# Performance work log

Hardware: AMD Instinct MI355X
Metric: run time of the kernel (lower is better)

## Reference

```python
import jax, jax.numpy as jnp
import numpy as np

N, C, T, V = 32, 64, 256, 25   # batch, channels, frames, joints
REL, OUT, K = 8, 64, 5         # rel_channels = C//8, out_channels, 5 topology branches
NU = 17                        # upper-body joints (lower = V - NU = 8)


def setup_inputs() -> dict:
    key = jax.random.key(0)
    ks = jax.random.split(key, 8)
    sC = np.float32(1.0 / np.sqrt(C))
    sR = np.float32(1.0 / np.sqrt(REL))
    return {
        "x": jax.random.normal(ks[0], (N, C, T, V), jnp.float32),
        "A": jax.random.uniform(ks[1], (K, V, V), jnp.float32),
        # stacked 1x1-conv weights for the 5 branches (conv{k}_1_1, _1_2, _2, _3, _4)
        "W11": jax.random.normal(ks[2], (K, REL, C), jnp.float32) * sC,
        "b11": jnp.zeros((K, REL), jnp.float32),
        "W12": jax.random.normal(ks[3], (K, REL, C), jnp.float32) * sC,
        "b12": jnp.zeros((K, REL), jnp.float32),
        "W2": jax.random.normal(ks[4], (K, REL, C), jnp.float32) * sC,
        "b2": jnp.zeros((K, REL), jnp.float32),
        "W3": jax.random.normal(ks[5], (K, OUT, C), jnp.float32) * sC,
        "b3": jnp.zeros((K, OUT), jnp.float32),
        "W4": jax.random.normal(ks[6], (K, OUT, REL), jnp.float32) * sR,
        "b4": jnp.zeros((K, OUT), jnp.float32),
    }


def reference(x, A, W11, b11, W12, b12, W2, b2, W3, b3, W4, b4):
    # 1x1 conv followed by mean over T commutes with the (linear) conv:
    # conv(x).mean(T) == W @ x.mean(T) + b. Pool once, reuse across branches.
    mu = jnp.mean(x[:, :, :, :NU], axis=2)   # (N, C, 17)
    ml = jnp.mean(x[:, :, :, NU:], axis=2)   # (N, C, 8)

    u11 = jnp.einsum('krc,ncv->knrv', W11, mu) + b11[:, None, :, None]  # (K,N,R,17)
    u2 = jnp.einsum('krc,ncv->knrv', W2, mu) + b2[:, None, :, None]     # (K,N,R,17)
    l12 = jnp.einsum('krc,ncv->knrv', W12, ml) + b12[:, None, :, None]  # (K,N,R,8)
    l2 = jnp.einsum('krc,ncv->knrv', W2, ml) + b2[:, None, :, None]     # (K,N,R,8)

    # pairwise-difference topology blocks
    x_a = jnp.tanh(u11[..., :, None] - u2[..., None, :])   # (K,N,R,17,17)
    x_b = jnp.tanh(u11[..., :, None] - l2[..., None, :])   # (K,N,R,17,8)
    x_c = jnp.tanh(l12[..., :, None] - u2[..., None, :])   # (K,N,R,8,17)
    x_d = jnp.tanh(l12[..., :, None] - l2[..., None, :])   # (K,N,R,8,8)

    up = jnp.concatenate([x_a, x_b], axis=-1)   # (K,N,R,17,25)
    lo = jnp.concatenate([x_c, x_d], axis=-1)   # (K,N,R,8,25)

    # the original rotates the upper blocks: branch k uses upper from branch (k+1)%5
    up_rot = jnp.concatenate([up[1:], up[:1]], axis=0)
    full = jnp.concatenate([up_rot, lo], axis=-2)  # (K,N,R,25,25)

    graphs = jnp.einsum('kor,knruv->knouv', W4, full) + b4[:, None, :, None, None]  # (K,N,O,25,25)

    alpha = jnp.ones((K,), jnp.float32)  # default branch scales
    g = graphs * alpha[:, None, None, None, None] + A[:, None, None, :, :]

    x2 = jnp.einsum('koc,nctv->knotv', W3, x) + b3[:, None, :, None, None]  # (K,N,O,T,25)
    out = jnp.einsum('knouv,knotv->notu', g, x2)  # summed over the 5 branches
    return out, graphs
```

## Files before the change

kernel.cpp:

```cpp
#include <hip/hip_runtime.h>
#include <cstdint>
#include <cstddef>

#define N_  32
#define C_  64
#define T_  256
#define V_  25
#define R_  8
#define O_  64
#define K_  5
#define NU_ 17
#define U_  25
#define CV  (C_ * V_)
#define KC  32
#define NCH (CV / KC)
#define OG  4
#define NB  (OG * 32)

#define OUT_ELEMS ((size_t)N_ * O_ * T_ * V_)

typedef __attribute__((ext_vector_type(8))) short bf16x8;
typedef __attribute__((ext_vector_type(4))) float f32x4;

static __device__ __forceinline__ unsigned short f2bf(float f) {
    union { float f; unsigned u; } c; c.f = f;
    return (unsigned short)((c.u + 0x8000u) >> 16);
}
static __device__ __forceinline__ float bf2f(unsigned short h) {
    union { unsigned u; float f; } c; c.u = ((unsigned)h) << 16; return c.f;
}
static __device__ __forceinline__ unsigned pk2(float a, float b) {
    union { float f; unsigned u; } ca, cb; ca.f = a; cb.f = b;
    return ((ca.u + 0x8000u) >> 16) | ((cb.u + 0x8000u) & 0xFFFF0000u);
}

__global__ void k_xcast(const float* __restrict__ x, unsigned short* __restrict__ xT3,
                        float* __restrict__ pp) {
    __shared__ unsigned short tile[C_][408];
    int bid = blockIdx.x;
    int n = bid >> 4, tb = bid & 15;
    int tid = threadIdx.x;
    const float* xb = x + (size_t)n * C_ * T_ * V_ + tb * 400;
#pragma unroll
    for (int it = 0; it < 25; ++it) {
        int i = it * 256 + tid;
        int c = i / 100, q = i - c * 100;
        float4 v4 = *(const float4*)(xb + (size_t)c * (T_ * V_) + q * 4);
        uint2 w;
        w.x = pk2(v4.x, v4.y);
        w.y = pk2(v4.z, v4.w);
        *(uint2*)&tile[c][q * 4] = w;
    }
    __syncthreads();
    unsigned short* dstb = xT3 + ((size_t)(n * 16 + tb) * 200) * 128;
    for (int i = tid; i < 200 * 16; i += 256) {
        int sp = i >> 4, tl = i & 15;
        int v = sp >> 3, c0 = (sp & 7) * 8;
        unsigned short h[8];
#pragma unroll
        for (int j = 0; j < 8; ++j) h[j] = tile[c0 + j][tl * 25 + v];
        uint4 pk;
        pk.x = (unsigned)h[0] | ((unsigned)h[1] << 16);
        pk.y = (unsigned)h[2] | ((unsigned)h[3] << 16);
        pk.z = (unsigned)h[4] | ((unsigned)h[5] << 16);
        pk.w = (unsigned)h[6] | ((unsigned)h[7] << 16);
        *(uint4*)(dstb + (size_t)sp * 128 + tl * 8) = pk;
    }
    float* ppd = pp + ((size_t)n * 16 + tb) * CV;
    for (int e = tid; e < CV; e += 256) {
        int c = e / 25, v = e - c * 25;
        float s = 0.f;
#pragma unroll
        for (int t = 0; t < 16; ++t) s += bf2f(tile[c][t * 25 + v]);
        ppd[e] = s;
    }
}

__global__ void k_pool(const float* __restrict__ x, float* __restrict__ pool) {
    int nc = blockIdx.x;
    int t  = threadIdx.x;
    const float* px = x + ((size_t)nc * T_ + t) * V_;
    float acc[V_];
#pragma unroll
    for (int v = 0; v < V_; ++v) acc[v] = px[v];
#pragma unroll
    for (int off = 32; off > 0; off >>= 1) {
#pragma unroll
        for (int v = 0; v < V_; ++v) acc[v] += __shfl_down(acc[v], off, 64);
    }
    __shared__ float sm[4][V_];
    int wave = t >> 6, lane = t & 63;
    if (lane == 0) {
#pragma unroll
        for (int v = 0; v < V_; ++v) sm[wave][v] = acc[v];
    }
    __syncthreads();
    if (t < V_) {
        float s = sm[0][t] + sm[1][t] + sm[2][t] + sm[3][t];
        pool[(size_t)nc * V_ + t] = s * (1.0f / T_);
    }
}

__global__ void k_tvals(const float* __restrict__ pool,
                        const float* __restrict__ W11, const float* __restrict__ b11,
                        const float* __restrict__ W12, const float* __restrict__ b12,
                        const float* __restrict__ W2,  const float* __restrict__ b2,
                        float* __restrict__ t2o, float* __restrict__ tSo) {
    int kn = blockIdx.x;
    int k = kn / N_, n = kn % N_;
    int tid = threadIdx.x;
    int r = tid >> 5, v = tid & 31;
    if (v >= V_) return;
    const float* pp = pool + (size_t)n * C_ * V_ + v;
    const float* w2 = W2 + ((size_t)k * R_ + r) * C_;
    const float* w1 = ((v < NU_) ? W11 : W12) + ((size_t)k * R_ + r) * C_;
    float a2 = b2[k * R_ + r];
    float a1 = (v < NU_) ? b11[k * R_ + r] : b12[k * R_ + r];
    for (int c = 0; c < C_; ++c) {
        float p = pp[(size_t)c * V_];
        a2 += w2[c] * p;
        a1 += w1[c] * p;
    }
    size_t idx = (((size_t)k * N_ + n) * R_ + r) * V_ + v;
    t2o[idx] = a2;
    tSo[idx] = a1;
}

__global__ void k_graphs(const float* __restrict__ t2v, const float* __restrict__ tSv,
                         const float* __restrict__ W4, const float* __restrict__ b4,
                         float* __restrict__ graphs) {
    int kn = blockIdx.x;
    int k = kn / N_, n = kn % N_;
    int kup = (k + 1) % K_;
    __shared__ float F[R_][V_ * V_];
    __shared__ float w4s[O_][R_];
    __shared__ float b4s[O_];
    int tid = threadIdx.x;
    for (int i = tid; i < O_ * R_; i += 256) w4s[i / R_][i % R_] = W4[(size_t)k * O_ * R_ + i];
    if (tid < O_) b4s[tid] = b4[k * O_ + tid];
    for (int idx = tid; idx < R_ * V_ * V_; idx += 256) {
        int r = idx / (V_ * V_), uv = idx % (V_ * V_);
        int u = uv / V_, v = uv % V_;
        int ks = (u < NU_) ? kup : k;
        size_t base = (((size_t)ks * N_ + n) * R_ + r) * V_;
        F[r][uv] = tanhf(tSv[base + u] - t2v[base + v]);
    }
    __syncthreads();
    float* gout = graphs + ((size_t)k * N_ + n) * O_ * (V_ * V_);
    for (int idx = tid; idx < O_ * V_ * V_; idx += 256) {
        int o = idx / (V_ * V_), uv = idx % (V_ * V_);
        float a = b4s[o];
#pragma unroll
        for (int r = 0; r < R_; ++r) a += w4s[o][r] * F[r][uv];
        gout[idx] = a;
    }
}

__global__ void k_graphs2b(const float* __restrict__ pp,
                           const float* __restrict__ W11, const float* __restrict__ b11,
                           const float* __restrict__ W12, const float* __restrict__ b12,
                           const float* __restrict__ W2,  const float* __restrict__ b2,
                           const float* __restrict__ W4,  const float* __restrict__ b4,
                           float* __restrict__ graphs) {
    int kn = blockIdx.x;
    int k = kn / N_, n = kn % N_;
    int kup = (k + 1) % K_;
    __shared__ float poolL[CV];
    __shared__ float t2s[2][R_][V_];
    __shared__ float tSs[2][R_][V_];
    __shared__ float F[R_][V_ * V_];
    __shared__ float w4s[O_][R_];
    __shared__ float b4s[O_];
    int tid = threadIdx.x;
    for (int i = tid; i < O_ * R_; i += 512) w4s[i / R_][i % R_] = W4[(size_t)k * O_ * R_ + i];
    if (tid < O_) b4s[tid] = b4[k * O_ + tid];
    const float* ppn = pp + (size_t)n * 16 * CV;
    for (int i = tid; i < CV; i += 512) {
        float s = 0.f;
#pragma unroll
        for (int tb = 0; tb < 16; ++tb) s += ppn[(size_t)tb * CV + i];
        poolL[i] = s * (1.0f / T_);
    }
    __syncthreads();
    for (int i = tid; i < 2 * R_ * V_; i += 512) {
        int ks = i / (R_ * V_);
        int rem = i - ks * (R_ * V_);
        int r = rem / V_, v = rem - r * V_;
        int kk = ks ? kup : k;
        const float* w2 = W2 + ((size_t)kk * R_ + r) * C_;
        const float* w1 = ((v < NU_) ? W11 : W12) + ((size_t)kk * R_ + r) * C_;
        float a2 = b2[kk * R_ + r];
        float a1 = (v < NU_) ? b11[kk * R_ + r] : b12[kk * R_ + r];
        for (int c = 0; c < C_; ++c) {
            float p = poolL[c * 25 + v];
            a2 += w2[c] * p;
            a1 += w1[c] * p;
        }
        t2s[ks][r][v] = a2;
        tSs[ks][r][v] = a1;
    }
    __syncthreads();
    for (int idx = tid; idx < R_ * V_ * V_; idx += 512) {
        int r = idx / (V_ * V_), uv = idx % (V_ * V_);
        int u = uv / V_, v = uv % V_;
        int ks = (u < NU_) ? 1 : 0;
        F[r][uv] = tanhf(tSs[ks][r][u] - t2s[ks][r][v]);
    }
    __syncthreads();
    float* gout = graphs + ((size_t)k * N_ + n) * O_ * (V_ * V_);
    for (int idx = tid; idx < O_ * V_ * V_; idx += 512) {
        int o = idx / (V_ * V_), uv = idx % (V_ * V_);
        float a = b4s[o];
#pragma unroll
        for (int r = 0; r < R_; ++r) a += w4s[o][r] * F[r][uv];
        gout[idx] = a;
    }
}

__global__ __launch_bounds__(512, 4) void k_main_fast(
    const unsigned short* __restrict__ xT3,
    const float* __restrict__ graphs,
    const float* __restrict__ Adj,
    const float* __restrict__ W3,
    const float* __restrict__ b3,
    float* __restrict__ out) {

    __shared__ unsigned short Hs[2][4][NB][8];
    __shared__ f32x4 Gls4[OG * 625];
    __shared__ float Gls1[OG * 625];
    __shared__ f32x4 W3km[K_ * OG * 16];
    __shared__ float biasS[NB];

    const int tid = threadIdx.x;
    const int bid = blockIdx.x;
    const int obase = (bid & 15) * OG;
    const int n = bid >> 4;
    const int lane = tid & 63;
    const int wv_ = tid >> 6;

    const size_t kstride = (size_t)N_ * O_ * 625;
    for (int i = tid; i < OG * 625; i += 512) {
        int o = i / 625, uv = i - o * 625;
        int u = uv / 25, v = uv - u * 25;
        size_t gb = ((size_t)n * O_ + obase + o) * 625 + uv;
        f32x4 g4;
        g4[0] = graphs[gb]               + Adj[uv];
        g4[1] = graphs[gb + kstride]     + Adj[625 + uv];
        g4[2] = graphs[gb + 2 * kstride] + Adj[1250 + uv];
        g4[3] = graphs[gb + 3 * kstride] + Adj[1875 + uv];
        int idx = o * 625 + v * 25 + u;
        Gls4[idx] = g4;
        Gls1[idx] = graphs[gb + 4 * kstride] + Adj[2500 + uv];
    }
    for (int i = tid; i < K_ * OG * C_; i += 512) {
        int k = i / (OG * C_);
        int rem = i - k * (OG * C_);
        int o = rem >> 6, c = rem & 63;
        ((float*)W3km)[((k * OG + o) * C_) + c] = W3[((size_t)k * O_ + obase + o) * C_ + c];
    }
    __syncthreads();

    if (tid < NB) {
        int o = tid >> 5, u = tid & 31;
        float bv = 0.f;
        if (u < U_) {
            f32x4 s4 = {0.f, 0.f, 0.f, 0.f};
            float s5 = 0.f;
            for (int v = 0; v < V_; ++v) {
                int idx = o * 625 + v * 25 + u;
                s4 += Gls4[idx];
                s5 += Gls1[idx];
            }
            bv = s4[0] * b3[0 * O_ + obase + o] + s4[1] * b3[1 * O_ + obase + o]
               + s4[2] * b3[2 * O_ + obase + o] + s4[3] * b3[3 * O_ + obase + o]
               + s5 * b3[4 * O_ + obase + o];
        }
        biasS[tid] = bv;
    }

    const int sl = wv_ & 3;
    const int hncol = (wv_ >> 2) * 64 + lane;
    const int ho = hncol >> 5;
    const int hu = hncol & 31;
    auto h_form = [&](int buf, int kc) {
        const int v  = kc >> 1;
        const int c0 = (kc & 1) * 32 + sl * 8;
        f32x4 g = {0.f, 0.f, 0.f, 0.f};
        float g5 = 0.f;
        if (hu < U_) {
            int gi = ho * 625 + v * 25 + hu;
            g = Gls4[gi];
            g5 = Gls1[gi];
        }
        const f32x4* wb = &W3km[(ho * 16) + (c0 >> 2)];
        const int kw = OG * 16;
        f32x4 w0a = wb[0],        w0b = wb[1];
        f32x4 w1a = wb[kw],       w1b = wb[kw + 1];
        f32x4 w2a = wb[2 * kw],   w2b = wb[2 * kw + 1];
        f32x4 w3a = wb[3 * kw],   w3b = wb[3 * kw + 1];
        f32x4 w4a = wb[4 * kw],   w4b = wb[4 * kw + 1];
        float h[8];
#pragma unroll
        for (int j = 0; j < 4; ++j) {
            h[j]     = w0a[j] * g[0] + w1a[j] * g[1] + w2a[j] * g[2] + w3a[j] * g[3] + w4a[j] * g5;
            h[4 + j] = w0b[j] * g[0] + w1b[j] * g[1] + w2b[j] * g[2] + w3b[j] * g[3] + w4b[j] * g5;
        }
        uint4 hv;
        hv.x = pk2(h[0], h[1]); hv.y = pk2(h[2], h[3]);
        hv.z = pk2(h[4], h[5]); hv.w = pk2(h[6], h[7]);
        *(uint4*)&Hs[buf][sl][hncol][0] = hv;
    };

    const int wm = wv_ >> 1;
    const int wn = wv_ & 1;
    const int lr = lane & 15;
    const int eg = lane >> 4;

    f32x4 acc[4][4];
#pragma unroll
    for (int mt = 0; mt < 4; ++mt)
#pragma unroll
        for (int nt = 0; nt < 4; ++nt) acc[mt][nt] = (f32x4){0.f, 0.f, 0.f, 0.f};

    h_form(0, 0);
    __syncthreads();

    const unsigned short* An = xT3 + (size_t)n * (T_ * CV);

    for (int kc = 0; kc < NCH; ++kc) {
        const int cur = kc & 1;
        uint4 av[4];
#pragma unroll
        for (int mt = 0; mt < 4; ++mt) {
            int tt = wm * 4 + mt;
            av[mt] = *(const uint4*)(An + ((size_t)(tt * 200 + kc * 4 + eg)) * 128 + lr * 8);
        }
        bf16x8 b[4];
#pragma unroll
        for (int nt = 0; nt < 4; ++nt)
            b[nt] = *(const bf16x8*)&Hs[cur][eg][wn * 64 + nt * 16 + lr][0];
        __builtin_amdgcn_s_setprio(1);
#pragma unroll
        for (int mt = 0; mt < 4; ++mt) {
            bf16x8 a;
            { union { uint4 u; bf16x8 h; } cvt; cvt.u = av[mt]; a = cvt.h; }
#pragma unroll
            for (int nt = 0; nt < 4; ++nt)
                acc[mt][nt] = __builtin_amdgcn_mfma_f32_16x16x32_bf16(a, b[nt], acc[mt][nt], 0, 0, 0);
        }
        __builtin_amdgcn_s_setprio(0);
        if (kc + 1 < NCH) h_form(cur ^ 1, kc + 1);
        __syncthreads();
    }

#pragma unroll
    for (int nt = 0; nt < 4; ++nt) {
        int ncol = wn * 64 + nt * 16 + lr;
        int ol = ncol >> 5;
        int u  = ncol & 31;
        if (u < U_) {
            float bv = biasS[ncol];
            float* ob = out + ((size_t)n * O_ + obase + ol) * T_ * V_ + u;
#pragma unroll
            for (int mt = 0; mt < 4; ++mt) {
                int t0 = wm * 64 + mt * 16 + eg * 4;
#pragma unroll
                for (int r2 = 0; r2 < 4; ++r2)
                    ob[(size_t)(t0 + r2) * V_] = acc[mt][nt][r2] + bv;
            }
        }
    }
}

#define OB 4
#define TB 64
__global__ __launch_bounds__(256, 1) void k_main_slow(
    const float* __restrict__ x, const float* __restrict__ graphs,
    const float* __restrict__ A, const float* __restrict__ W3,
    const float* __restrict__ b3, float* __restrict__ out) {
    int bid = blockIdx.x;
    int tb = bid & 3;
    int ob = (bid >> 2) & 15;
    int n  = bid >> 6;
    int tid = threadIdx.x;
    int ol = tid >> 6;
    int tl = tid & 63;
    int t = tb * TB + tl;
    int o = ob * OB + ol;

    __shared__ float Gs[K_][OB][V_][28];
    __shared__ float W3s[K_][OB][C_];
    __shared__ float b3s[K_][OB];

    for (int i = tid; i < K_ * OB * V_ * V_; i += 256) {
        int k   = i / (OB * V_ * V_);
        int rem = i % (OB * V_ * V_);
        int oo  = rem / (V_ * V_);
        int uv  = rem % (V_ * V_);
        Gs[k][oo][uv / V_][uv % V_] =
            graphs[(((size_t)k * N_ + n) * O_ + ob * OB + oo) * (V_ * V_) + uv]
            + A[k * V_ * V_ + uv];
    }
    for (int i = tid; i < K_ * OB * C_; i += 256) {
        int k   = i / (OB * C_);
        int rem = i % (OB * C_);
        int oo  = rem / C_, c = rem % C_;
        W3s[k][oo][c] = W3[((size_t)k * O_ + ob * OB + oo) * C_ + c];
    }
    if (tid < K_ * OB) b3s[tid / OB][tid % OB] = b3[(tid / OB) * O_ + ob * OB + tid % OB];
    __syncthreads();

    float x2[K_][V_];
#pragma unroll
    for (int k = 0; k < K_; ++k)
#pragma unroll
        for (int v = 0; v < V_; ++v) x2[k][v] = b3s[k][ol];

    const float* xb = x + ((size_t)n * C_ * T_ + t) * V_;
    for (int c = 0; c < C_; ++c) {
        const float* p = xb + (size_t)c * T_ * V_;
        float xv[V_];
#pragma unroll
        for (int v = 0; v < V_; ++v) xv[v] = p[v];
#pragma unroll
        for (int k = 0; k < K_; ++k) {
            float w = W3s[k][ol][c];
#pragma unroll
            for (int v = 0; v < V_; ++v) x2[k][v] += w * xv[v];
        }
    }

    float acc[V_];
#pragma unroll
    for (int u = 0; u < V_; ++u) acc[u] = 0.0f;
#pragma unroll
    for (int k = 0; k < K_; ++k) {
#pragma unroll
        for (int u = 0; u < V_; ++u) {
            const float* gr = &Gs[k][ol][u][0];
            float s = 0.0f;
#pragma unroll
            for (int v = 0; v < V_; ++v) s += gr[v] * x2[k][v];
            acc[u] += s;
        }
    }
    float* po = out + (((size_t)n * O_ + o) * T_ + t) * V_;
#pragma unroll
    for (int u = 0; u < V_; ++u) po[u] = acc[u];
}

extern "C" void kernel_launch(void* const* d_in, const int* in_sizes, int n_in,
                              void* d_out, int out_size, void* d_ws, size_t ws_size,
                              hipStream_t stream) {
    const float* x   = (const float*)d_in[0];
    const float* A   = (const float*)d_in[1];
    const float* W11 = (const float*)d_in[2];
    const float* b11 = (const float*)d_in[3];
    const float* W12 = (const float*)d_in[4];
    const float* b12 = (const float*)d_in[5];
    const float* W2  = (const float*)d_in[6];
    const float* b2  = (const float*)d_in[7];
    const float* W3  = (const float*)d_in[8];
    const float* b3  = (const float*)d_in[9];
    const float* W4  = (const float*)d_in[10];
    const float* b4  = (const float*)d_in[11];

    float* out    = (float*)d_out;
    float* graphs = out + OUT_ELEMS;

    const size_t xT_bytes = sizeof(unsigned short) * (size_t)N_ * T_ * CV;
    const size_t pp_bytes = sizeof(float) * (size_t)N_ * 16 * CV;
    const size_t hdr      = (size_t)(1 << 20);
    const bool fast = (ws_size >= hdr + xT_bytes + pp_bytes);

    const size_t poolElems = (size_t)N_ * C_ * V_;
    const size_t tElems    = (size_t)K_ * N_ * R_ * V_;
    const size_t slowNeed  = (poolElems + 2 * tElems) * sizeof(float);

    float* scratch = (fast || ws_size >= slowNeed) ? (float*)d_ws : out;
    float* pool = scratch;
    float* t2v  = scratch + poolElems;
    float* tSv  = t2v + tElems;
    unsigned short* xT3 = (unsigned short*)((char*)d_ws + hdr);
    float* pp = (float*)((char*)d_ws + hdr + xT_bytes);

    if (fast) {
        k_xcast   <<<N_ * 16, 256, 0, stream>>>(x, xT3, pp);
        k_graphs2b<<<K_ * N_, 512, 0, stream>>>(pp, W11, b11, W12, b12, W2, b2, W4, b4, graphs);
        k_main_fast<<<N_ * 16, 512, 0, stream>>>(xT3, graphs, A, W3, b3, out);
    } else {
        k_pool  <<<N_ * C_, 256, 0, stream>>>(x, pool);
        k_tvals <<<K_ * N_, 256, 0, stream>>>(pool, W11, b11, W12, b12, W2, b2, t2v, tSv);
        k_graphs<<<K_ * N_, 256, 0, stream>>>(t2v, tSv, W4, b4, graphs);
        k_main_slow<<<N_ * (O_ / OB) * 4, 256, 0, stream>>>(x, graphs, A, W3, b3, out);
    }
}
```

Measured before the change: 116.1 us.

## Process two K-chunks per barrier with quad-buffered H and bf16 graphs in LDS

The main GEMM loop now handles two joint chunks between barriers, using four H slots instead of two. This cuts the number of __syncthreads from about 50 to 26 per block. The combined graph+adjacency tiles are stored in LDS as packed bf16 rather than fp32, which halves that footprint to make room for the larger H buffer. The cost is an extra rounding of G to bf16 before H is formed, with a small accuracy risk, plus some unpacking ALU work.

```diff
diff --git a/kernel.cpp b/kernel.cpp
--- a/kernel.cpp
+++ b/kernel.cpp
@@ -12,8 +12,6 @@
 #define NU_ 17
 #define U_  25
 #define CV  (C_ * V_)
-#define KC  32
-#define NCH (CV / KC)
 #define OG  4
 #define NB  (OG * 32)
 
@@ -28,6 +26,12 @@
 }
 static __device__ __forceinline__ float bf2f(unsigned short h) {
     union { unsigned u; float f; } c; c.u = ((unsigned)h) << 16; return c.f;
+}
+static __device__ __forceinline__ float bf_lo(unsigned d) {
+    union { unsigned u; float f; } c; c.u = d << 16; return c.f;
+}
+static __device__ __forceinline__ float bf_hi(unsigned d) {
+    union { unsigned u; float f; } c; c.u = d & 0xFFFF0000u; return c.f;
 }
 static __device__ __forceinline__ unsigned pk2(float a, float b) {
     union { float f; unsigned u; } ca, cb; ca.f = a; cb.f = b;
@@ -225,9 +229,9 @@
     const float* __restrict__ b3,
     float* __restrict__ out) {
 
-    __shared__ unsigned short Hs[2][4][NB][8];
-    __shared__ f32x4 Gls4[OG * 625];
-    __shared__ float Gls1[OG * 625];
+    __shared__ unsigned short Hs[4][4][NB][8];
+    __shared__ uint2 Gbf4[OG * 625];
+    __shared__ unsigned short Gbf1[OG * 625];
     __shared__ f32x4 W3km[K_ * OG * 16];
     __shared__ float biasS[NB];
 
@@ -243,14 +247,15 @@
         int o = i / 625, uv = i - o * 625;
         int u = uv / 25, v = uv - u * 25;
         size_t gb = ((size_t)n * O_ + obase + o) * 625 + uv;
-        f32x4 g4;
-        g4[0] = graphs[gb]               + Adj[uv];
-        g4[1] = graphs[gb + kstride]     + Adj[625 + uv];
-        g4[2] = graphs[gb + 2 * kstride] + Adj[1250 + uv];
-        g4[3] = graphs[gb + 3 * kstride] + Adj[1875 + uv];
+        float g0 = graphs[gb]               + Adj[uv];
+        float g1 = graphs[gb + kstride]     + Adj[625 + uv];
+        float g2 = graphs[gb + 2 * kstride] + Adj[1250 + uv];
+        float g3 = graphs[gb + 3 * kstride] + Adj[1875 + uv];
+        float g4 = graphs[gb + 4 * kstride] + Adj[2500 + uv];
         int idx = o * 625 + v * 25 + u;
-        Gls4[idx] = g4;
-        Gls1[idx] = graphs[gb + 4 * kstride] + Adj[2500 + uv];
+        uint2 w; w.x = pk2(g0, g1); w.y = pk2(g2, g3);
+        Gbf4[idx] = w;
+        Gbf1[idx] = f2bf(g4);
     }
     for (int i = tid; i < K_ * OG * C_; i += 512) {
         int k = i / (OG * C_);
@@ -264,16 +269,17 @@
         int o = tid >> 5, u = tid & 31;
         float bv = 0.f;
         if (u < U_) {
-            f32x4 s4 = {0.f, 0.f, 0.f, 0.f};
-            float s5 = 0.f;
+            float s0 = 0.f, s1 = 0.f, s2 = 0.f, s3 = 0.f, s4 = 0.f;
             for (int v = 0; v < V_; ++v) {
                 int idx = o * 625 + v * 25 + u;
-                s4 += Gls4[idx];
-                s5 += Gls1[idx];
+                uint2 w = Gbf4[idx];
+                s0 += bf_lo(w.x); s1 += bf_hi(w.x);
+                s2 += bf_lo(w.y); s3 += bf_hi(w.y);
+                s4 += bf2f(Gbf1[idx]);
             }
-            bv = s4[0] * b3[0 * O_ + obase + o] + s4[1] * b3[1 * O_ + obase + o]
-               + s4[2] * b3[2 * O_ + obase + o] + s4[3] * b3[3 * O_ + obase + o]
-               + s5 * b3[4 * O_ + obase + o];
+            bv = s0 * b3[0 * O_ + obase + o] + s1 * b3[1 * O_ + obase + o]
+               + s2 * b3[2 * O_ + obase + o] + s3 * b3[3 * O_ + obase + o]
+               + s4 * b3[4 * O_ + obase + o];
         }
         biasS[tid] = bv;
     }
@@ -282,33 +288,40 @@
     const int hncol = (wv_ >> 2) * 64 + lane;
     const int ho = hncol >> 5;
     const int hu = hncol & 31;
-    auto h_form = [&](int buf, int kc) {
-        const int v  = kc >> 1;
-        const int c0 = (kc & 1) * 32 + sl * 8;
-        f32x4 g = {0.f, 0.f, 0.f, 0.f};
-        float g5 = 0.f;
-        if (hu < U_) {
-            int gi = ho * 625 + v * 25 + hu;
-            g = Gls4[gi];
-            g5 = Gls1[gi];
-        }
+    const int kw = OG * 16;
+    auto h_form_pair = [&](int i) {
+        const int par = i & 1;
+        const int vb  = (i < 24) ? ((i >> 1) * 2) : 24;
+        const int nv  = (i < 24) ? 2 : 1;
+        const int csb = (i & 1) * 2;
+        const int c0  = par * 32 + sl * 8;
         const f32x4* wb = &W3km[(ho * 16) + (c0 >> 2)];
-        const int kw = OG * 16;
         f32x4 w0a = wb[0],        w0b = wb[1];
         f32x4 w1a = wb[kw],       w1b = wb[kw + 1];
         f32x4 w2a = wb[2 * kw],   w2b = wb[2 * kw + 1];
         f32x4 w3a = wb[3 * kw],   w3b = wb[3 * kw + 1];
         f32x4 w4a = wb[4 * kw],   w4b = wb[4 * kw + 1];
-        float h[8];
-#pragma unroll
-        for (int j = 0; j < 4; ++j) {
-            h[j]     = w0a[j] * g[0] + w1a[j] * g[1] + w2a[j] * g[2] + w3a[j] * g[3] + w4a[j] * g5;
-            h[4 + j] = w0b[j] * g[0] + w1b[j] * g[1] + w2b[j] * g[2] + w3b[j] * g[3] + w4b[j] * g5;
-        }
-        uint4 hv;
-        hv.x = pk2(h[0], h[1]); hv.y = pk2(h[2], h[3]);
-        hv.z = pk2(h[4], h[5]); hv.w = pk2(h[6], h[7]);
-        *(uint4*)&Hs[buf][sl][hncol][0] = hv;
+        for (int vi = 0; vi < nv; ++vi) {
+            const int v = vb + vi;
+            float g0 = 0.f, g1 = 0.f, g2 = 0.f, g3 = 0.f, g4 = 0.f;
+            if (hu < U_) {
+                int gi = ho * 625 + v * 25 + hu;
+                uint2 gw = Gbf4[gi];
+                g0 = bf_lo(gw.x); g1 = bf_hi(gw.x);
+                g2 = bf_lo(gw.y); g3 = bf_hi(gw.y);
+                g4 = bf2f(Gbf1[gi]);
+            }
+            float h[8];
+#pragma unroll
+            for (int j = 0; j < 4; ++j) {
+                h[j]     = w0a[j] * g0 + w1a[j] * g1 + w2a[j] * g2 + w3a[j] * g3 + w4a[j] * g4;
+                h[4 + j] = w0b[j] * g0 + w1b[j] * g1 + w2b[j] * g2 + w3b[j] * g3 + w4b[j] * g4;
+            }
+            uint4 hv;
+            hv.x = pk2(h[0], h[1]); hv.y = pk2(h[2], h[3]);
+            hv.z = pk2(h[4], h[5]); hv.w = pk2(h[6], h[7]);
+            *(uint4*)&Hs[csb + vi][sl][hncol][0] = hv;
+        }
     };
 
     const int wm = wv_ >> 1;
@@ -322,23 +335,19 @@
 #pragma unroll
         for (int nt = 0; nt < 4; ++nt) acc[mt][nt] = (f32x4){0.f, 0.f, 0.f, 0.f};
 
-    h_form(0, 0);
-    __syncthreads();
-
     const unsigned short* An = xT3 + (size_t)n * (T_ * CV);
 
-    for (int kc = 0; kc < NCH; ++kc) {
-        const int cur = kc & 1;
+    auto consume = [&](int v, int par, int cs) {
         uint4 av[4];
 #pragma unroll
         for (int mt = 0; mt < 4; ++mt) {
             int tt = wm * 4 + mt;
-            av[mt] = *(const uint4*)(An + ((size_t)(tt * 200 + kc * 4 + eg)) * 128 + lr * 8);
+            av[mt] = *(const uint4*)(An + ((size_t)(tt * 200 + v * 8 + par * 4 + eg)) * 128 + lr * 8);
         }
         bf16x8 b[4];
 #pragma unroll
         for (int nt = 0; nt < 4; ++nt)
-            b[nt] = *(const bf16x8*)&Hs[cur][eg][wn * 64 + nt * 16 + lr][0];
+            b[nt] = *(const bf16x8*)&Hs[cs][eg][wn * 64 + nt * 16 + lr][0];
         __builtin_amdgcn_s_setprio(1);
 #pragma unroll
         for (int mt = 0; mt < 4; ++mt) {
@@ -349,7 +358,19 @@
                 acc[mt][nt] = __builtin_amdgcn_mfma_f32_16x16x32_bf16(a, b[nt], acc[mt][nt], 0, 0, 0);
         }
         __builtin_amdgcn_s_setprio(0);
-        if (kc + 1 < NCH) h_form(cur ^ 1, kc + 1);
+    };
+
+    h_form_pair(0);
+    __syncthreads();
+
+    for (int i = 0; i < 26; ++i) {
+        const int par = i & 1;
+        const int vb  = (i < 24) ? ((i >> 1) * 2) : 24;
+        const int nv  = (i < 24) ? 2 : 1;
+        const int csb = (i & 1) * 2;
+        consume(vb, par, csb);
+        if (nv == 2) consume(vb + 1, par, csb + 1);
+        if (i + 1 < 26) h_form_pair(i + 1);
         __syncthreads();
     }
 
```

Result: slower. 196.0 us (+68.8%).

## Unroll main GEMM loop by two, use hardware bf16 pack, split graph kernel

Applied to the files above, without the earlier changes.

The main MFMA loop is manually unrolled over pairs of K chunks. Global pointers for A are precomputed and the G values are loaded once per joint instead of once per chunk, which cuts address arithmetic and redundant LDS reads. The software bf16 rounding is replaced by the v_cvt_pk_bf16_f32 instruction, which may change rounding slightly on ties or NaN. The graph kernel now launches twice as many blocks, each writing half the output channels, for more parallelism at the cost of recomputing the pooled and tanh stages in both blocks.

```diff
diff --git a/kernel.cpp b/kernel.cpp
--- a/kernel.cpp
+++ b/kernel.cpp
@@ -12,8 +12,6 @@
 #define NU_ 17
 #define U_  25
 #define CV  (C_ * V_)
-#define KC  32
-#define NCH (CV / KC)
 #define OG  4
 #define NB  (OG * 32)
 
@@ -32,6 +30,11 @@
 static __device__ __forceinline__ unsigned pk2(float a, float b) {
     union { float f; unsigned u; } ca, cb; ca.f = a; cb.f = b;
     return ((ca.u + 0x8000u) >> 16) | ((cb.u + 0x8000u) & 0xFFFF0000u);
+}
+static __device__ __forceinline__ unsigned cvtpk(float a, float b) {
+    unsigned r;
+    asm("v_cvt_pk_bf16_f32 %0, %1, %2" : "=v"(r) : "v"(a), "v"(b));
+    return r;
 }
 
 __global__ void k_xcast(const float* __restrict__ x, unsigned short* __restrict__ xT3,
@@ -156,13 +159,15 @@
     }
 }
 
-__global__ void k_graphs2b(const float* __restrict__ pp,
+__global__ void k_graphs2c(const float* __restrict__ pp,
                            const float* __restrict__ W11, const float* __restrict__ b11,
                            const float* __restrict__ W12, const float* __restrict__ b12,
                            const float* __restrict__ W2,  const float* __restrict__ b2,
                            const float* __restrict__ W4,  const float* __restrict__ b4,
                            float* __restrict__ graphs) {
-    int kn = blockIdx.x;
+    int bid = blockIdx.x;
+    int og = bid & 1;
+    int kn = bid >> 1;
     int k = kn / N_, n = kn % N_;
     int kup = (k + 1) % K_;
     __shared__ float poolL[CV];
@@ -208,7 +213,8 @@
     }
     __syncthreads();
     float* gout = graphs + ((size_t)k * N_ + n) * O_ * (V_ * V_);
-    for (int idx = tid; idx < O_ * V_ * V_; idx += 512) {
+    const int half = O_ * V_ * V_ / 2;
+    for (int idx = og * half + tid; idx < (og + 1) * half; idx += 512) {
         int o = idx / (V_ * V_), uv = idx % (V_ * V_);
         float a = b4s[o];
 #pragma unroll
@@ -282,23 +288,18 @@
     const int hncol = (wv_ >> 2) * 64 + lane;
     const int ho = hncol >> 5;
     const int hu = hncol & 31;
-    auto h_form = [&](int buf, int kc) {
-        const int v  = kc >> 1;
-        const int c0 = (kc & 1) * 32 + sl * 8;
-        f32x4 g = {0.f, 0.f, 0.f, 0.f};
-        float g5 = 0.f;
-        if (hu < U_) {
-            int gi = ho * 625 + v * 25 + hu;
-            g = Gls4[gi];
-            g5 = Gls1[gi];
-        }
-        const f32x4* wb = &W3km[(ho * 16) + (c0 >> 2)];
-        const int kw = OG * 16;
-        f32x4 w0a = wb[0],        w0b = wb[1];
-        f32x4 w1a = wb[kw],       w1b = wb[kw + 1];
-        f32x4 w2a = wb[2 * kw],   w2b = wb[2 * kw + 1];
-        f32x4 w3a = wb[3 * kw],   w3b = wb[3 * kw + 1];
-        f32x4 w4a = wb[4 * kw],   w4b = wb[4 * kw + 1];
+    const int kw = OG * 16;
+    const f32x4* wb  = &W3km[ho * 16 + sl * 2];
+    const f32x4* gp4 = &Gls4[ho * 625 + hu];
+    const float* gp1 = &Gls1[ho * 625 + hu];
+    uint4* hw = (uint4*)&Hs[0][sl][hncol][0];
+
+    auto h_form = [&](uint4* hwp, const f32x4* wbp, f32x4 g, float g5) {
+        f32x4 w0a = wbp[0],        w0b = wbp[1];
+        f32x4 w1a = wbp[kw],       w1b = wbp[kw + 1];
+        f32x4 w2a = wbp[2 * kw],   w2b = wbp[2 * kw + 1];
+        f32x4 w3a = wbp[3 * kw],   w3b = wbp[3 * kw + 1];
+        f32x4 w4a = wbp[4 * kw],   w4b = wbp[4 * kw + 1];
         float h[8];
 #pragma unroll
         for (int j = 0; j < 4; ++j) {
@@ -306,9 +307,13 @@
             h[4 + j] = w0b[j] * g[0] + w1b[j] * g[1] + w2b[j] * g[2] + w3b[j] * g[3] + w4b[j] * g5;
         }
         uint4 hv;
-        hv.x = pk2(h[0], h[1]); hv.y = pk2(h[2], h[3]);
-        hv.z = pk2(h[4], h[5]); hv.w = pk2(h[6], h[7]);
-        *(uint4*)&Hs[buf][sl][hncol][0] = hv;
+        hv.x = cvtpk(h[0], h[1]); hv.y = cvtpk(h[2], h[3]);
+        hv.z = cvtpk(h[4], h[5]); hv.w = cvtpk(h[6], h[7]);
+        *hwp = hv;
+    };
+    auto ld_g = [&](int voff25, f32x4& g, float& g5) {
+        if (hu < U_) { g = gp4[voff25]; g5 = gp1[voff25]; }
+        else { g = (f32x4){0.f, 0.f, 0.f, 0.f}; g5 = 0.f; }
     };
 
     const int wm = wv_ >> 1;
@@ -322,35 +327,52 @@
 #pragma unroll
         for (int nt = 0; nt < 4; ++nt) acc[mt][nt] = (f32x4){0.f, 0.f, 0.f, 0.f};
 
-    h_form(0, 0);
-    __syncthreads();
-
     const unsigned short* An = xT3 + (size_t)n * (T_ * CV);
-
-    for (int kc = 0; kc < NCH; ++kc) {
-        const int cur = kc & 1;
-        uint4 av[4];
-#pragma unroll
-        for (int mt = 0; mt < 4; ++mt) {
-            int tt = wm * 4 + mt;
-            av[mt] = *(const uint4*)(An + ((size_t)(tt * 200 + kc * 4 + eg)) * 128 + lr * 8);
-        }
+    const unsigned short* a0 = An + ((size_t)((wm * 4 + 0) * 200 + eg)) * 128 + lr * 8;
+    const unsigned short* a1 = a0 + 200 * 128;
+    const unsigned short* a2 = a0 + 400 * 128;
+    const unsigned short* a3 = a0 + 600 * 128;
+    const char* hrb = (const char*)&Hs[0][eg][wn * 64 + lr][0];
+
+    auto consume = [&](int sub , int bufb ) {
+        uint4 av0 = *(const uint4*)(a0 + sub);
+        uint4 av1 = *(const uint4*)(a1 + sub);
+        uint4 av2 = *(const uint4*)(a2 + sub);
+        uint4 av3 = *(const uint4*)(a3 + sub);
         bf16x8 b[4];
 #pragma unroll
         for (int nt = 0; nt < 4; ++nt)
-            b[nt] = *(const bf16x8*)&Hs[cur][eg][wn * 64 + nt * 16 + lr][0];
+            b[nt] = *(const bf16x8*)(hrb + bufb + nt * 256);
         __builtin_amdgcn_s_setprio(1);
-#pragma unroll
-        for (int mt = 0; mt < 4; ++mt) {
-            bf16x8 a;
-            { union { uint4 u; bf16x8 h; } cvt; cvt.u = av[mt]; a = cvt.h; }
-#pragma unroll
-            for (int nt = 0; nt < 4; ++nt)
-                acc[mt][nt] = __builtin_amdgcn_mfma_f32_16x16x32_bf16(a, b[nt], acc[mt][nt], 0, 0, 0);
-        }
+        union { uint4 u; bf16x8 h; } c0, c1, c2, c3;
+        c0.u = av0; c1.u = av1; c2.u = av2; c3.u = av3;
+#pragma unroll
+        for (int nt = 0; nt < 4; ++nt) acc[0][nt] = __builtin_amdgcn_mfma_f32_16x16x32_bf16(c0.h, b[nt], acc[0][nt], 0, 0, 0);
+#pragma unroll
+        for (int nt = 0; nt < 4; ++nt) acc[1][nt] = __builtin_amdgcn_mfma_f32_16x16x32_bf16(c1.h, b[nt], acc[1][nt], 0, 0, 0);
+#pragma unroll
+        for (int nt = 0; nt < 4; ++nt) acc[2][nt] = __builtin_amdgcn_mfma_f32_16x16x32_bf16(c2.h, b[nt], acc[2][nt], 0, 0, 0);
+#pragma unroll
+        for (int nt = 0; nt < 4; ++nt) acc[3][nt] = __builtin_amdgcn_mfma_f32_16x16x32_bf16(c3.h, b[nt], acc[3][nt], 0, 0, 0);
         __builtin_amdgcn_s_setprio(0);
-        if (kc + 1 < NCH) h_form(cur ^ 1, kc + 1);
+    };
+
+    f32x4 gv; float gv5;
+    ld_g(0, gv, gv5);
+    h_form(hw, wb, gv, gv5);
+    __syncthreads();
+
+    for (int kc2 = 0; kc2 < 25; ++kc2) {
+        consume(0, 0);
+        h_form(hw + 512, wb + 8, gv, gv5);
         __syncthreads();
+        consume(512, 8192);
+        if (kc2 + 1 < 25) {
+            ld_g((kc2 + 1) * 25, gv, gv5);
+            h_form(hw, wb, gv, gv5);
+        }
+        __syncthreads();
+        a0 += 1024; a1 += 1024; a2 += 1024; a3 += 1024;
     }
 
 #pragma unroll
@@ -486,7 +508,7 @@
 
     if (fast) {
         k_xcast   <<<N_ * 16, 256, 0, stream>>>(x, xT3, pp);
-        k_graphs2b<<<K_ * N_, 512, 0, stream>>>(pp, W11, b11, W12, b12, W2, b2, W4, b4, graphs);
+        k_graphs2c<<<K_ * N_ * 2, 512, 0, stream>>>(pp, W11, b11, W12, b12, W2, b2, W4, b4, graphs);
         k_main_fast<<<N_ * 16, 512, 0, stream>>>(xT3, graphs, A, W3, b3, out);
     } else {
         k_pool  <<<N_ * C_, 256, 0, stream>>>(x, pool);
```

After: 110.9 us. 1.05x faster.

## Reassociate main GEMM: apply W3 to x first, then graph contraction per tile

Applied to the files above, without the earlier changes.

The main kernel used to fold W3 into the graph (H = G·W3) and contract over all C×V in one long K loop per (n, 4 output channels). It now computes x2 = W3·x per small (n, 2 channels, 64-frame) tile with MFMA, stores x2 and the transposed graph+A in swizzled bf16 LDS, and runs a short K=125 MFMA against the graph. The grid grows from 512 to 4096 smaller 256-thread blocks with a swizzled block order, and the graphs kernel is split into two blocks per (k,n) to add parallelism. The price is that x is re-read for every channel-pair block, W3·x is recomputed across output groups, and padded MFMA columns are wasted.

```diff
diff --git a/kernel.cpp b/kernel.cpp
--- a/kernel.cpp
+++ b/kernel.cpp
@@ -12,10 +12,8 @@
 #define NU_ 17
 #define U_  25
 #define CV  (C_ * V_)
-#define KC  32
-#define NCH (CV / KC)
-#define OG  4
-#define NB  (OG * 32)
+#define OG  2
+#define TBLK 64
 
 #define OUT_ELEMS ((size_t)N_ * O_ * T_ * V_)
 
@@ -32,6 +30,9 @@
 static __device__ __forceinline__ unsigned pk2(float a, float b) {
     union { float f; unsigned u; } ca, cb; ca.f = a; cb.f = b;
     return ((ca.u + 0x8000u) >> 16) | ((cb.u + 0x8000u) & 0xFFFF0000u);
+}
+static __device__ __forceinline__ bf16x8 asbf(uint4 u) {
+    union { uint4 u; bf16x8 h; } c; c.u = u; return c.h;
 }
 
 __global__ void k_xcast(const float* __restrict__ x, unsigned short* __restrict__ xT3,
@@ -156,13 +157,15 @@
     }
 }
 
-__global__ void k_graphs2b(const float* __restrict__ pp,
+__global__ void k_graphs2c(const float* __restrict__ pp,
                            const float* __restrict__ W11, const float* __restrict__ b11,
                            const float* __restrict__ W12, const float* __restrict__ b12,
                            const float* __restrict__ W2,  const float* __restrict__ b2,
                            const float* __restrict__ W4,  const float* __restrict__ b4,
                            float* __restrict__ graphs) {
-    int kn = blockIdx.x;
+    int bid = blockIdx.x;
+    int og = bid & 1;
+    int kn = bid >> 1;
     int k = kn / N_, n = kn % N_;
     int kup = (k + 1) % K_;
     __shared__ float poolL[CV];
@@ -208,7 +211,8 @@
     }
     __syncthreads();
     float* gout = graphs + ((size_t)k * N_ + n) * O_ * (V_ * V_);
-    for (int idx = tid; idx < O_ * V_ * V_; idx += 512) {
+    const int half = O_ * V_ * V_ / 2;
+    for (int idx = og * half + tid; idx < (og + 1) * half; idx += 512) {
         int o = idx / (V_ * V_), uv = idx % (V_ * V_);
         float a = b4s[o];
 #pragma unroll
@@ -217,7 +221,7 @@
     }
 }
 
-__global__ __launch_bounds__(512, 4) void k_main_fast(
+__global__ __launch_bounds__(256, 3) void k_main_fast(
     const unsigned short* __restrict__ xT3,
     const float* __restrict__ graphs,
     const float* __restrict__ Adj,
@@ -225,148 +229,131 @@
     const float* __restrict__ b3,
     float* __restrict__ out) {
 
-    __shared__ unsigned short Hs[2][4][NB][8];
-    __shared__ f32x4 Gls4[OG * 625];
-    __shared__ float Gls1[OG * 625];
-    __shared__ f32x4 W3km[K_ * OG * 16];
-    __shared__ float biasS[NB];
+    __shared__ unsigned short x2s[OG][TBLK][128];
+    __shared__ unsigned short GtL[OG][32][128];
+    __shared__ unsigned short W3L[16][64];
+    __shared__ float biasS[OG][32];
 
     const int tid = threadIdx.x;
-    const int bid = blockIdx.x;
-    const int obase = (bid & 15) * OG;
-    const int n = bid >> 4;
+    int raw = blockIdx.x;
+    int bidn = (raw & 7) * 512 + (raw >> 3);
+    const int og = bidn & 31;
+    const int tb = (bidn >> 5) & 3;
+    const int n  = bidn >> 7;
+    const int obase = og * OG;
+    const int tgb = tb * TBLK;
     const int lane = tid & 63;
     const int wv_ = tid >> 6;
-
-    const size_t kstride = (size_t)N_ * O_ * 625;
-    for (int i = tid; i < OG * 625; i += 512) {
-        int o = i / 625, uv = i - o * 625;
-        int u = uv / 25, v = uv - u * 25;
-        size_t gb = ((size_t)n * O_ + obase + o) * 625 + uv;
-        f32x4 g4;
-        g4[0] = graphs[gb]               + Adj[uv];
-        g4[1] = graphs[gb + kstride]     + Adj[625 + uv];
-        g4[2] = graphs[gb + 2 * kstride] + Adj[1250 + uv];
-        g4[3] = graphs[gb + 3 * kstride] + Adj[1875 + uv];
-        int idx = o * 625 + v * 25 + u;
-        Gls4[idx] = g4;
-        Gls1[idx] = graphs[gb + 4 * kstride] + Adj[2500 + uv];
-    }
-    for (int i = tid; i < K_ * OG * C_; i += 512) {
-        int k = i / (OG * C_);
-        int rem = i - k * (OG * C_);
-        int o = rem >> 6, c = rem & 63;
-        ((float*)W3km)[((k * OG + o) * C_) + c] = W3[((size_t)k * O_ + obase + o) * C_ + c];
-    }
-    __syncthreads();
-
-    if (tid < NB) {
-        int o = tid >> 5, u = tid & 31;
-        float bv = 0.f;
-        if (u < U_) {
-            f32x4 s4 = {0.f, 0.f, 0.f, 0.f};
-            float s5 = 0.f;
-            for (int v = 0; v < V_; ++v) {
-                int idx = o * 625 + v * 25 + u;
-                s4 += Gls4[idx];
-                s5 += Gls1[idx];
-            }
-            bv = s4[0] * b3[0 * O_ + obase + o] + s4[1] * b3[1 * O_ + obase + o]
-               + s4[2] * b3[2 * O_ + obase + o] + s4[3] * b3[3 * O_ + obase + o]
-               + s5 * b3[4 * O_ + obase + o];
-        }
-        biasS[tid] = bv;
-    }
-
-    const int sl = wv_ & 3;
-    const int hncol = (wv_ >> 2) * 64 + lane;
-    const int ho = hncol >> 5;
-    const int hu = hncol & 31;
-    auto h_form = [&](int buf, int kc) {
-        const int v  = kc >> 1;
-        const int c0 = (kc & 1) * 32 + sl * 8;
-        f32x4 g = {0.f, 0.f, 0.f, 0.f};
-        float g5 = 0.f;
-        if (hu < U_) {
-            int gi = ho * 625 + v * 25 + hu;
-            g = Gls4[gi];
-            g5 = Gls1[gi];
-        }
-        const f32x4* wb = &W3km[(ho * 16) + (c0 >> 2)];
-        const int kw = OG * 16;
-        f32x4 w0a = wb[0],        w0b = wb[1];
-        f32x4 w1a = wb[kw],       w1b = wb[kw + 1];
-        f32x4 w2a = wb[2 * kw],   w2b = wb[2 * kw + 1];
-        f32x4 w3a = wb[3 * kw],   w3b = wb[3 * kw + 1];
-        f32x4 w4a = wb[4 * kw],   w4b = wb[4 * kw + 1];
-        float h[8];
-#pragma unroll
-        for (int j = 0; j < 4; ++j) {
-            h[j]     = w0a[j] * g[0] + w1a[j] * g[1] + w2a[j] * g[2] + w3a[j] * g[3] + w4a[j] * g5;
-            h[4 + j] = w0b[j] * g[0] + w1b[j] * g[1] + w2b[j] * g[2] + w3b[j] * g[3] + w4b[j] * g5;
-        }
-        uint4 hv;
-        hv.x = pk2(h[0], h[1]); hv.y = pk2(h[2], h[3]);
-        hv.z = pk2(h[4], h[5]); hv.w = pk2(h[6], h[7]);
-        *(uint4*)&Hs[buf][sl][hncol][0] = hv;
-    };
-
-    const int wm = wv_ >> 1;
-    const int wn = wv_ & 1;
     const int lr = lane & 15;
     const int eg = lane >> 4;
 
-    f32x4 acc[4][4];
-#pragma unroll
-    for (int mt = 0; mt < 4; ++mt)
-#pragma unroll
-        for (int nt = 0; nt < 4; ++nt) acc[mt][nt] = (f32x4){0.f, 0.f, 0.f, 0.f};
-
-    h_form(0, 0);
-    __syncthreads();
-
-    const unsigned short* An = xT3 + (size_t)n * (T_ * CV);
-
-    for (int kc = 0; kc < NCH; ++kc) {
-        const int cur = kc & 1;
-        uint4 av[4];
-#pragma unroll
-        for (int mt = 0; mt < 4; ++mt) {
-            int tt = wm * 4 + mt;
-            av[mt] = *(const uint4*)(An + ((size_t)(tt * 200 + kc * 4 + eg)) * 128 + lr * 8);
-        }
-        bf16x8 b[4];
-#pragma unroll
-        for (int nt = 0; nt < 4; ++nt)
-            b[nt] = *(const bf16x8*)&Hs[cur][eg][wn * 64 + nt * 16 + lr][0];
-        __builtin_amdgcn_s_setprio(1);
-#pragma unroll
-        for (int mt = 0; mt < 4; ++mt) {
-            bf16x8 a;
-            { union { uint4 u; bf16x8 h; } cvt; cvt.u = av[mt]; a = cvt.h; }
-#pragma unroll
-            for (int nt = 0; nt < 4; ++nt)
-                acc[mt][nt] = __builtin_amdgcn_mfma_f32_16x16x32_bf16(a, b[nt], acc[mt][nt], 0, 0, 0);
-        }
-        __builtin_amdgcn_s_setprio(0);
-        if (kc + 1 < NCH) h_form(cur ^ 1, kc + 1);
-        __syncthreads();
-    }
-
-#pragma unroll
-    for (int nt = 0; nt < 4; ++nt) {
-        int ncol = wn * 64 + nt * 16 + lr;
-        int ol = ncol >> 5;
-        int u  = ncol & 31;
-        if (u < U_) {
-            float bv = biasS[ncol];
-            float* ob = out + ((size_t)n * O_ + obase + ol) * T_ * V_ + u;
-#pragma unroll
-            for (int mt = 0; mt < 4; ++mt) {
-                int t0 = wm * 64 + mt * 16 + eg * 4;
-#pragma unroll
-                for (int r2 = 0; r2 < 4; ++r2)
-                    ob[(size_t)(t0 + r2) * V_] = acc[mt][nt][r2] + bv;
+    {
+        uint4 z; z.x = z.y = z.z = z.w = 0u;
+        for (int i = tid; i < (OG * TBLK * 128) / 8; i += 256) ((uint4*)x2s)[i] = z;
+        for (int i = tid; i < (OG * 32 * 128) / 8; i += 256) ((uint4*)GtL)[i] = z;
+        if (tid < 48) ((uint4*)&W3L[10][0])[tid] = z;
+        for (int i = tid; i < 10 * C_; i += 256) {
+            int ncol = i >> 6, c = i & 63;
+            int k = ncol >> 1, o = ncol & 1;
+            W3L[ncol][c] = f2bf(W3[((size_t)k * O_ + obase + o) * C_ + c]);
+        }
+    }
+    __syncthreads();
+
+    const size_t kstride = (size_t)N_ * O_ * 625;
+    if (tid < OG * K_ * 25) {
+        int o = tid / 125;
+        int rem = tid - o * 125;
+        int k = rem / 25, u = rem - k * 25;
+        const float* gp = graphs + (size_t)k * kstride + ((size_t)n * O_ + obase + o) * 625 + u * 25;
+        const float* ap = Adj + k * 625 + u * 25;
+        char* rowb = (char*)GtL + (o * 32 + u) * 256;
+        const int swz = (u & 7) << 4;
+#pragma unroll
+        for (int v = 0; v < V_; ++v) {
+            float g = gp[v] + ap[v];
+            *(unsigned short*)(rowb + (((k * 25 + v) * 2) ^ swz)) = f2bf(g);
+        }
+    }
+
+    {
+        bf16x8 wb0 = *(const bf16x8*)&W3L[lr][eg * 8];
+        bf16x8 wb1 = *(const bf16x8*)&W3L[lr][32 + eg * 8];
+        const unsigned short* Axb = xT3 + (size_t)n * (T_ * CV);
+        const int kA = (lr < 10) ? (lr >> 1) : 0;
+        const int oA = lr & 1;
+        for (int i = 0; i < 25; ++i) {
+            int mt = wv_ * 25 + i;
+            int row = mt * 16 + lr;
+            int t = (row * 5243) >> 17;
+            int v = row - t * 25;
+            int tg = tgb + t;
+            const unsigned short* pA = Axb + ((size_t)((tg >> 4) * 200 + v * 8 + eg)) * 128 + (tg & 15) * 8;
+            uint4 a0 = *(const uint4*)pA;
+            uint4 a1 = *(const uint4*)(pA + 4 * 128);
+            f32x4 acc = {0.f, 0.f, 0.f, 0.f};
+            acc = __builtin_amdgcn_mfma_f32_16x16x32_bf16(asbf(a0), wb0, acc, 0, 0, 0);
+            acc = __builtin_amdgcn_mfma_f32_16x16x32_bf16(asbf(a1), wb1, acc, 0, 0, 0);
+            if (lr < 10) {
+#pragma unroll
+                for (int r2 = 0; r2 < 4; ++r2) {
+                    int rw = mt * 16 + eg * 4 + r2;
+                    int tw = (rw * 5243) >> 17;
+                    int vw = rw - tw * 25;
+                    int byte = (oA * TBLK + tw) * 256 + ((((kA * 25 + vw) * 2)) ^ ((tw & 7) << 4));
+                    *(unsigned short*)((char*)x2s + byte) = f2bf(acc[r2]);
+                }
+            }
+        }
+    }
+    __syncthreads();
+
+    if (tid < OG * 25) {
+        int o = tid / 25, u = tid - o * 25;
+        const char* rowb = (const char*)GtL + (o * 32 + u) * 256;
+        const int swz = (u & 7) << 4;
+        float bv = 0.f;
+#pragma unroll
+        for (int k = 0; k < K_; ++k) {
+            float sk = 0.f;
+            for (int v = 0; v < V_; ++v)
+                sk += bf2f(*(const unsigned short*)(rowb + (((k * 25 + v) * 2) ^ swz)));
+            bv += sk * b3[k * O_ + obase + o];
+        }
+        biasS[o][u] = bv;
+    }
+    __syncthreads();
+
+#pragma unroll
+    for (int uu = 0; uu < 2; ++uu) {
+        int unit = wv_ * 2 + uu;
+        int o = unit >> 2, mt = unit & 3;
+        int t = mt * 16 + lr;
+        f32x4 acc0 = {0.f, 0.f, 0.f, 0.f};
+        f32x4 acc1 = {0.f, 0.f, 0.f, 0.f};
+        const int aswz = (t & 7) << 4;
+        const int bswz = (lr & 7) << 4;
+#pragma unroll
+        for (int ks = 0; ks < 4; ++ks) {
+            int col = ks * 64 + eg * 16;
+            bf16x8 a  = *(const bf16x8*)((const char*)x2s + (o * TBLK + t) * 256 + (col ^ aswz));
+            bf16x8 b0 = *(const bf16x8*)((const char*)GtL + (o * 32 + lr) * 256 + (col ^ bswz));
+            bf16x8 b1 = *(const bf16x8*)((const char*)GtL + (o * 32 + 16 + lr) * 256 + (col ^ bswz));
+            acc0 = __builtin_amdgcn_mfma_f32_16x16x32_bf16(a, b0, acc0, 0, 0, 0);
+            acc1 = __builtin_amdgcn_mfma_f32_16x16x32_bf16(a, b1, acc1, 0, 0, 0);
+        }
+        float* ob = out + ((size_t)n * O_ + obase + o) * T_ * V_;
+#pragma unroll
+        for (int nt = 0; nt < 2; ++nt) {
+            f32x4 ac = nt ? acc1 : acc0;
+            int u = nt * 16 + lr;
+            if (u < U_) {
+                float bv = biasS[o][u];
+#pragma unroll
+                for (int r2 = 0; r2 < 4; ++r2) {
+                    int tl2 = mt * 16 + eg * 4 + r2;
+                    ob[(size_t)(tgb + tl2) * V_ + u] = ac[r2] + bv;
+                }
             }
         }
     }
@@ -486,8 +473,8 @@
 
     if (fast) {
         k_xcast   <<<N_ * 16, 256, 0, stream>>>(x, xT3, pp);
-        k_graphs2b<<<K_ * N_, 512, 0, stream>>>(pp, W11, b11, W12, b12, W2, b2, W4, b4, graphs);
-        k_main_fast<<<N_ * 16, 512, 0, stream>>>(xT3, graphs, A, W3, b3, out);
+        k_graphs2c<<<K_ * N_ * 2, 512, 0, stream>>>(pp, W11, b11, W12, b12, W2, b2, W4, b4, graphs);
+        k_main_fast<<<N_ * 4 * (O_ / OG), 256, 0, stream>>>(xT3, graphs, A, W3, b3, out);
     } else {
         k_pool  <<<N_ * C_, 256, 0, stream>>>(x, pool);
         k_tvals <<<K_ * N_, 256, 0, stream>>>(pool, W11, b11, W12, b12, W2, b2, t2v, tSv);
```

After: 259.4 us. +123.4%, slower.
